# Kernel optimization log

Hardware: AMD Instinct MI355X
Metric: run time of the kernel (lower is better)

## Reference

```python
import jax, jax.numpy as jnp
import numpy as np

K = 7          # involution kernel size
PAD = 3        # (K-1)//2
G = 4          # groups = out_channels // group_channels
GC = 16        # group_channels
EPS = 1e-5     # BatchNorm eps


def _bn(x, g, b, m, v):
    # eval-mode BatchNorm2d over channel dim of NCHW
    scale = g / jnp.sqrt(v + EPS)
    return x * scale[:, None, None] + (b - m * scale)[:, None, None]


def _conv1x1(x, w, b=None):
    y = jnp.einsum('bchw,oc->bohw', x, w)
    if b is not None:
        y = y + b[:, None, None]
    return y


def _gelu(x):
    return jax.nn.gelu(x, approximate=False)  # torch nn.GELU default (erf)


def _involution(x, wr, gr, br, mr, vr, ws, bs):
    # kernel-generation branch: 1x1 reduce -> BN -> ReLU -> 1x1 span
    r = jax.nn.relu(_bn(_conv1x1(x, wr), gr, br, mr, vr))
    w = _conv1x1(r, ws, bs)                       # [B, G*K*K, H, W]
    B, _, H, W = w.shape
    w = w.reshape(B, G, K * K, H, W)
    # unfold x into KxK patches (channel-major then row-major kernel pos, matching nn.Unfold)
    xp = jnp.pad(x, ((0, 0), (0, 0), (PAD, PAD), (PAD, PAD)))
    patches = jnp.stack([xp[:, :, i:i + H, j:j + W]
                         for i in range(K) for j in range(K)], axis=2)  # [B, C, KK, H, W]
    patches = patches.reshape(B, G, GC, K * K, H, W)
    out = jnp.einsum('bgkhw,bgckhw->bgchw', w, patches)  # per-pixel dynamic kernel apply
    return out.reshape(B, G * GC, H, W)


def setup_inputs() -> dict:
    key = jax.random.key(0)
    ks = jax.random.split(key, 24)
    B, Cin, Cout, H, W = 4, 32, 64, 128, 128
    red = Cout // 4
    n = lambda k, s, sc: jax.random.normal(k, s, jnp.float32) * sc
    u = lambda k, s: jax.random.uniform(k, s, jnp.float32, 0.5, 1.5)
    inp = {
        'x': n(ks[0], (B, Cin, H, W), 1.0),
        'w1': n(ks[1], (Cout, Cin), 0.15),
        # involution: reduce conv + BN, span conv
        'wr': n(ks[2], (red, Cout), 0.12), 'gr': u(ks[3], (red,)), 'br': n(ks[4], (red,), 0.05),
        'mr': n(ks[5], (red,), 0.05), 'vr': u(ks[6], (red,)),
        'ws': n(ks[7], (K * K * G, red), 0.1), 'bs': n(ks[8], (K * K * G,), 0.02),
        # BN after involution
        'g1': u(ks[9], (Cout,)), 'b1': n(ks[10], (Cout,), 0.05),
        'm1': n(ks[11], (Cout,), 0.05), 'v1': u(ks[12], (Cout,)),
        # convblock2
        'w2': n(ks[13], (Cout, Cout), 0.12),
        'g2': u(ks[14], (Cout,)), 'b2': n(ks[15], (Cout,), 0.05),
        'm2': n(ks[16], (Cout,), 0.05), 'v2': u(ks[17], (Cout,)),
        # mapping (residual projection) conv has bias=True by default
        'wm': n(ks[18], (Cout, Cin), 0.15), 'bmap': n(ks[19], (Cout,), 0.02),
        'gm': u(ks[20], (Cout,)), 'betam': n(ks[21], (Cout,), 0.05),
        'mm': n(ks[22], (Cout,), 0.05), 'vm': u(ks[23], (Cout,)),
    }
    return inp


def reference(x, w1, wr, gr, br, mr, vr, ws, bs, g1, b1, m1, v1,
              w2, g2, b2, m2, v2, wm, bmap, gm, betam, mm, vm):
    x1 = _gelu(_conv1x1(x, w1))                                  # convblock
    x1 = _gelu(_bn(_involution(x1, wr, gr, br, mr, vr, ws, bs),
                   g1, b1, m1, v1))                              # involution + BN + GELU
    x1 = _bn(_conv1x1(x1, w2), g2, b2, m2, v2)                   # convblock2
    skip = _bn(_conv1x1(x, wm, bmap), gm, betam, mm, vm)         # mapping (Cin != Cout)
    return _gelu(x1 + skip)
```

## Files before the change

### kernel.cpp

```cpp
#include <hip/hip_runtime.h>
#include <hip/hip_bf16.h>
#include <math.h>

#define HW    16384
#define Bsz   4
#define CIN   32
#define COUT  64
#define RED   16
#define KKN   49
#define GG    4
#define PW    134
#define PPLANE (PW*PW)
#define N16PAD 574592

typedef __hip_bfloat16 bf16;
typedef __attribute__((ext_vector_type(8))) short bf16x8;
typedef __attribute__((ext_vector_type(4))) float f32x4;

__device__ __forceinline__ float gelu_f(float x) {
    return 0.5f * x * (1.0f + erff(x * 0.70710678118654752f));
}
__device__ __forceinline__ void unpack_bf2(unsigned u, float& lo, float& hi) {
    lo = __uint_as_float(u << 16);
    hi = __uint_as_float(u & 0xffff0000u);
}
__device__ __forceinline__ unsigned pack_bf2(float lo, float hi) {
    unsigned a = __float_as_uint(lo), b = __float_as_uint(hi);
    a += 0x7fff + ((a >> 16) & 1);
    b += 0x7fff + ((b >> 16) & 1);
    return (a >> 16) | (b & 0xffff0000u);
}
__device__ __forceinline__ unsigned short bf16r(float v) {
    unsigned a = __float_as_uint(v);
    a += 0x7fff + ((a >> 16) & 1);
    return (unsigned short)(a >> 16);
}

#define OFF_RBUF  9437184
#define OFF_X2B   13631488
#define OFF_PAR   22020096
#define OFF_XBF   22085632
#define PRSH_F 0
#define PSHC_F 16
#define PSMV_F 80
#define PSC1_F 144
#define PSH1_F 208
#define BW1B 4096
#define BWRB 8192
#define BCAT 12288

__global__ __launch_bounds__(256) void k0_init(
    const float* __restrict__ x,
    const float* __restrict__ w1, const float* __restrict__ wr,
    const float* __restrict__ gr, const float* __restrict__ br,
    const float* __restrict__ mr, const float* __restrict__ vr,
    const float* __restrict__ g1, const float* __restrict__ b1,
    const float* __restrict__ m1, const float* __restrict__ v1,
    const float* __restrict__ w2, const float* __restrict__ g2,
    const float* __restrict__ b2, const float* __restrict__ m2,
    const float* __restrict__ v2,
    const float* __restrict__ wm, const float* __restrict__ bmap,
    const float* __restrict__ gm, const float* __restrict__ betam,
    const float* __restrict__ mm, const float* __restrict__ vm,
    char* __restrict__ parb, uint4* __restrict__ x1pad,
    unsigned short* __restrict__ xbf, int nzb)
{
    int bid = blockIdx.x, t = threadIdx.x;
    if (bid >= 1 && bid <= nzb) {
        int i = (bid - 1) * 256 + t;
        if (i < N16PAD) x1pad[i] = make_uint4(0u, 0u, 0u, 0u);
        return;
    }
    if (bid > nzb) {
        int gpx = (bid - nzb - 1) * 256 + t;
        int b = gpx >> 14, p = gpx & (HW - 1);
        float xv[CIN];
#pragma unroll
        for (int c = 0; c < CIN; ++c) xv[c] = x[(b * CIN + c) * HW + p];
        unsigned pk[16];
#pragma unroll
        for (int d = 0; d < 16; ++d) pk[d] = pack_bf2(xv[2 * d], xv[2 * d + 1]);
        unsigned* xo = (unsigned*)&xbf[(size_t)gpx * 32];
        *(uint4*)xo        = make_uint4(pk[0], pk[1], pk[2], pk[3]);
        *(uint4*)(xo + 4)  = make_uint4(pk[4], pk[5], pk[6], pk[7]);
        *(uint4*)(xo + 8)  = make_uint4(pk[8], pk[9], pk[10], pk[11]);
        *(uint4*)(xo + 12) = make_uint4(pk[12], pk[13], pk[14], pk[15]);
        return;
    }
    float* parf = (float*)parb;
    unsigned short* w1b  = (unsigned short*)(parb + BW1B);
    unsigned short* wrb  = (unsigned short*)(parb + BWRB);
    unsigned short* wcat = (unsigned short*)(parb + BCAT);
    for (int i = t; i < 64 * 32; i += 256)
        w1b[i] = bf16r(w1[i]);
    for (int i = t; i < 16 * 64; i += 256) {
        int j = i >> 6;
        float sc = gr[j] * rsqrtf(vr[j] + 1e-5f);
        wrb[i] = bf16r(wr[i] * sc);
    }
    for (int i = t; i < 64 * 96; i += 256) {
        int o = i / 96, c = i - o * 96;
        float v;
        if (c < 64) {
            float s2 = g2[o] * rsqrtf(v2[o] + 1e-5f);
            float sm = gm[o] * rsqrtf(vm[o] + 1e-5f);
            v = w2[o * COUT + c] * (s2 / sm);
        } else {
            v = wm[o * CIN + (c - 64)];
        }
        wcat[i] = bf16r(v);
    }
    if (t < 16) {
        float sc = gr[t] * rsqrtf(vr[t] + 1e-5f);
        parf[PRSH_F + t] = br[t] - mr[t] * sc;
    }
    if (t < 64) {
        float s2 = g2[t] * rsqrtf(v2[t] + 1e-5f);
        float sm = gm[t] * rsqrtf(vm[t] + 1e-5f);
        parf[PSHC_F + t] = (b2[t] - m2[t] * s2) + (betam[t] + (bmap[t] - mm[t]) * sm);
        parf[PSMV_F + t] = sm;
        float s1 = g1[t] * rsqrtf(v1[t] + 1e-5f);
        parf[PSC1_F + t] = s1;
        parf[PSH1_F + t] = b1[t] - m1[t] * s1;
    }
}

__global__ __launch_bounds__(256, 4) void k1_mfma(
    const unsigned short* __restrict__ xbf, const char* __restrict__ parb,
    unsigned* __restrict__ x1pad, float* __restrict__ rbuf)
{
    __shared__ float x1f[4][16][65];

    int lane = threadIdx.x & 63;
    int wave = threadIdx.x >> 6;
    int m15 = lane & 15, quad = lane >> 4;
    int base_gpx = blockIdx.x * 64 + wave * 16;
    int b   = base_gpx >> 14;
    int px0 = base_gpx & (HW - 1);

    const unsigned short* w1b = (const unsigned short*)(parb + BW1B);
    const unsigned short* wrb = (const unsigned short*)(parb + BWRB);
    const float* parf = (const float*)parb;

    bf16x8 Af = *(const bf16x8*)&xbf[((size_t)(base_gpx + m15)) * 32 + quad * 8];
    f32x4 acc[4];
#pragma unroll
    for (int nt = 0; nt < 4; ++nt) {
        bf16x8 Bf = *(const bf16x8*)&w1b[(nt * 16 + m15) * 32 + quad * 8];
        f32x4 z = {0.f, 0.f, 0.f, 0.f};
        acc[nt] = __builtin_amdgcn_mfma_f32_16x16x32_bf16(Af, Bf, z, 0, 0, 0);
    }
#pragma unroll
    for (int nt = 0; nt < 4; ++nt)
#pragma unroll
        for (int reg = 0; reg < 4; ++reg)
            x1f[wave][quad * 4 + reg][nt * 16 + m15] = gelu_f(acc[nt][reg]);

    __syncthreads();

    {
        int pxl = lane >> 2, g = lane & 3;
        int p = px0 + pxl, h = p >> 7, w = p & 127;
        unsigned pk[8];
#pragma unroll
        for (int d = 0; d < 8; ++d)
            pk[d] = pack_bf2(x1f[wave][pxl][g * 16 + 2 * d],
                             x1f[wave][pxl][g * 16 + 2 * d + 1]);
        unsigned* xo = x1pad +
            ((size_t)((b * GG + g) * PW + (h + 3)) * PW + (w + 3)) * 8;
        *(uint4*)xo       = make_uint4(pk[0], pk[1], pk[2], pk[3]);
        *(uint4*)(xo + 4) = make_uint4(pk[4], pk[5], pk[6], pk[7]);
    }

    f32x4 racc = {0.f, 0.f, 0.f, 0.f};
#pragma unroll
    for (int kt = 0; kt < 2; ++kt) {
        bf16x8 A2, B2;
#pragma unroll
        for (int j = 0; j < 8; ++j)
            A2[j] = (short)bf16r(x1f[wave][m15][kt * 32 + quad * 8 + j]);
        B2 = *(const bf16x8*)&wrb[m15 * 64 + kt * 32 + quad * 8];
        racc = __builtin_amdgcn_mfma_f32_16x16x32_bf16(A2, B2, racc, 0, 0, 0);
    }
    float rsh = parf[PRSH_F + m15];
#pragma unroll
    for (int reg = 0; reg < 4; ++reg) {
        int gp = base_gpx + quad * 4 + reg;
        rbuf[(size_t)gp * 16 + m15] = fmaxf(racc[reg] + rsh, 0.f);
    }
}

__global__ __launch_bounds__(256, 4) void k23_involution(
    const unsigned* __restrict__ x1pad, const float* __restrict__ rbuf,
    const float* __restrict__ wsp, const float* __restrict__ bsp,
    const float* __restrict__ par, unsigned* __restrict__ x2b)
{
    int bg = blockIdx.x >> 6;
    int g = bg & 3, b = bg >> 2;
    int p = ((blockIdx.x & 63) << 8) + threadIdx.x;
    int h = p >> 7, w0 = p & 127;

    float r[RED];
    {
        const float4* rp = (const float4*)&rbuf[((size_t)b * HW + p) * 16];
        float4 r0 = rp[0], r1 = rp[1], r2 = rp[2], r3 = rp[3];
        r[0]=r0.x; r[1]=r0.y; r[2]=r0.z; r[3]=r0.w;
        r[4]=r1.x; r[5]=r1.y; r[6]=r1.z; r[7]=r1.w;
        r[8]=r2.x; r[9]=r2.y; r[10]=r2.z; r[11]=r2.w;
        r[12]=r3.x; r[13]=r3.y; r[14]=r3.z; r[15]=r3.w;
    }

    const float* wrow = wsp + g * KKN * RED;
    const float* brow = bsp + g * KKN;
    const unsigned* base = x1pad + ((size_t)(bg * PW + h) * PW + w0) * 8;

    float acc[RED];
#pragma unroll
    for (int c = 0; c < RED; ++c) acc[c] = 0.f;

#pragma unroll 1
    for (int i = 0; i < 7; ++i) {
#pragma unroll 1
        for (int j = 0; j < 7; ++j) {
            int k = i * 7 + j;
            const float* wk_row = wrow + k * RED;
            float s = brow[k];
#pragma unroll
            for (int jj = 0; jj < RED; ++jj) s += r[jj] * wk_row[jj];
            const unsigned* tp = base + (size_t)(i * PW + j) * 8;
            uint4 A = *(const uint4*)tp;
            uint4 B = *(const uint4*)(tp + 4);
            float lo, hi;
            unpack_bf2(A.x, lo, hi); acc[0] += s*lo; acc[1] += s*hi;
            unpack_bf2(A.y, lo, hi); acc[2] += s*lo; acc[3] += s*hi;
            unpack_bf2(A.z, lo, hi); acc[4] += s*lo; acc[5] += s*hi;
            unpack_bf2(A.w, lo, hi); acc[6] += s*lo; acc[7] += s*hi;
            unpack_bf2(B.x, lo, hi); acc[8] += s*lo; acc[9] += s*hi;
            unpack_bf2(B.y, lo, hi); acc[10]+= s*lo; acc[11]+= s*hi;
            unpack_bf2(B.z, lo, hi); acc[12]+= s*lo; acc[13]+= s*hi;
            unpack_bf2(B.w, lo, hi); acc[14]+= s*lo; acc[15]+= s*hi;
        }
    }

    unsigned pk[8];
#pragma unroll
    for (int d = 0; d < 8; ++d) {
        int ch0 = g * RED + 2 * d, ch1 = ch0 + 1;
        float v0 = gelu_f(par[PSC1_F + ch0] * acc[2 * d]     + par[PSH1_F + ch0]);
        float v1 = gelu_f(par[PSC1_F + ch1] * acc[2 * d + 1] + par[PSH1_F + ch1]);
        pk[d] = pack_bf2(v0, v1);
    }
    unsigned* xo = x2b + ((size_t)bg * HW + p) * 8;
    *(uint4*)xo       = make_uint4(pk[0], pk[1], pk[2], pk[3]);
    *(uint4*)(xo + 4) = make_uint4(pk[4], pk[5], pk[6], pk[7]);
}

__global__ __launch_bounds__(256, 4) void k4_mfma(
    const unsigned short* __restrict__ x2s, const unsigned short* __restrict__ xbf,
    const char* __restrict__ parb, float* __restrict__ out)
{
    int lane = threadIdx.x & 63;
    int wave = threadIdx.x >> 6;
    int m15  = lane & 15;
    int quad = lane >> 4;
    int b    = blockIdx.x >> 8;
    int px0  = (((blockIdx.x & 255) << 2) + wave) << 4;

    const unsigned short* wcat = (const unsigned short*)(parb + BCAT);
    const float* parf = (const float*)parb;

    bf16x8 Bf[3][4];
#pragma unroll
    for (int kt = 0; kt < 3; ++kt)
#pragma unroll
        for (int nt = 0; nt < 4; ++nt)
            Bf[kt][nt] = *(const bf16x8*)&wcat[(nt * 16 + m15) * 96 + kt * 32 + quad * 8];

    int px = px0 + m15;
    bf16x8 Af[3];
    {
        int g0 = quad >> 1, co = (quad & 1) * 8;
        Af[0] = *(const bf16x8*)&x2s[((size_t)((b * 4 + g0) * HW + px)) * 16 + co];
        Af[1] = *(const bf16x8*)&x2s[((size_t)((b * 4 + 2 + g0) * HW + px)) * 16 + co];
        Af[2] = *(const bf16x8*)&xbf[((size_t)(b * HW + px)) * 32 + quad * 8];
    }

    f32x4 acc[4];
#pragma unroll
    for (int nt = 0; nt < 4; ++nt) acc[nt] = (f32x4){0.f, 0.f, 0.f, 0.f};
#pragma unroll
    for (int kt = 0; kt < 3; ++kt)
#pragma unroll
        for (int nt = 0; nt < 4; ++nt)
            acc[nt] = __builtin_amdgcn_mfma_f32_16x16x32_bf16(
                Af[kt], Bf[kt][nt], acc[nt], 0, 0, 0);

#pragma unroll
    for (int nt = 0; nt < 4; ++nt) {
        int o = nt * 16 + m15;
        float smv = parf[PSMV_F + o], sh = parf[PSHC_F + o];
        float* op = out + (size_t)(b * COUT + o) * HW + px0 + quad * 4;
#pragma unroll
        for (int reg = 0; reg < 4; ++reg)
            op[reg] = gelu_f(smv * acc[nt][reg] + sh);
    }
}

extern "C" void kernel_launch(void* const* d_in, const int* in_sizes, int n_in,
                              void* d_out, int out_size, void* d_ws, size_t ws_size,
                              hipStream_t stream) {
    const float* x    = (const float*)d_in[0];
    const float* w1   = (const float*)d_in[1];
    const float* wr   = (const float*)d_in[2];
    const float* gr   = (const float*)d_in[3];
    const float* br   = (const float*)d_in[4];
    const float* mr   = (const float*)d_in[5];
    const float* vr   = (const float*)d_in[6];
    const float* wsp  = (const float*)d_in[7];
    const float* bsp  = (const float*)d_in[8];
    const float* g1   = (const float*)d_in[9];
    const float* b1   = (const float*)d_in[10];
    const float* m1   = (const float*)d_in[11];
    const float* v1   = (const float*)d_in[12];
    const float* w2   = (const float*)d_in[13];
    const float* g2   = (const float*)d_in[14];
    const float* b2   = (const float*)d_in[15];
    const float* m2   = (const float*)d_in[16];
    const float* v2   = (const float*)d_in[17];
    const float* wm   = (const float*)d_in[18];
    const float* bmap = (const float*)d_in[19];
    const float* gm   = (const float*)d_in[20];
    const float* betam= (const float*)d_in[21];
    const float* mm   = (const float*)d_in[22];
    const float* vm   = (const float*)d_in[23];

    unsigned*       x1pad = (unsigned*)d_ws;
    float*          rbuf  = (float*)((char*)d_ws + OFF_RBUF);
    unsigned*       x2b   = (unsigned*)((char*)d_ws + OFF_X2B);
    char*           parb  = (char*)d_ws + OFF_PAR;
    unsigned short* xbf   = (unsigned short*)((char*)d_ws + OFF_XBF);

    int nzb = (N16PAD + 255) / 256;
    int nxb = Bsz * HW / 256;
    k0_init<<<1 + nzb + nxb, 256, 0, stream>>>(
        x, w1, wr, gr, br, mr, vr, g1, b1, m1, v1,
        w2, g2, b2, m2, v2, wm, bmap, gm, betam, mm, vm,
        parb, (uint4*)x1pad, xbf, nzb);
    k1_mfma<<<Bsz * HW / 64, 256, 0, stream>>>(xbf, parb, x1pad, rbuf);
    k23_involution<<<Bsz * GG * HW / 256, 256, 0, stream>>>(
        x1pad, rbuf, wsp, bsp, (const float*)parb, x2b);
    k4_mfma<<<Bsz * HW / 64, 256, 0, stream>>>(
        (const unsigned short*)x2b, xbf, parb, (float*)d_out);
}
```

Measured before the change: 170.8 us.

## Fuse involution with final 1x1 conv via LDS and zero only halo

```diff
diff --git a/kernel.cpp b/kernel.cpp
--- a/kernel.cpp
+++ b/kernel.cpp
@@ -11,7 +11,7 @@
 #define GG    4
 #define PW    134
 #define PPLANE (PW*PW)
-#define N16PAD 574592
+#define NHALO 25152
 
 typedef __hip_bfloat16 bf16;
 typedef __attribute__((ext_vector_type(8))) short bf16x8;
@@ -67,8 +67,26 @@
 {
     int bid = blockIdx.x, t = threadIdx.x;
     if (bid >= 1 && bid <= nzb) {
-        int i = (bid - 1) * 256 + t;
-        if (i < N16PAD) x1pad[i] = make_uint4(0u, 0u, 0u, 0u);
+        unsigned i = (unsigned)(bid - 1) * 256u + (unsigned)t;
+        if (i < NHALO) {
+            unsigned plane = i / 1572u;
+            unsigned rem = i - plane * 1572u;
+            unsigned row, col;
+            if (rem < 804u) {
+                unsigned rr = rem / 134u;
+                col = rem - rr * 134u;
+                row = rr < 3u ? rr : rr + 128u;
+            } else {
+                unsigned r2 = rem - 804u;
+                unsigned rr = r2 / 6u;
+                unsigned cc = r2 - rr * 6u;
+                row = rr + 3u;
+                col = cc < 3u ? cc : cc + 128u;
+            }
+            uint4* q = x1pad + ((size_t)(plane * PW + row) * PW + col) * 2;
+            q[0] = make_uint4(0u, 0u, 0u, 0u);
+            q[1] = make_uint4(0u, 0u, 0u, 0u);
+        }
         return;
     }
     if (bid > nzb) {
@@ -190,119 +208,123 @@
     }
 }
 
-__global__ __launch_bounds__(256, 4) void k23_involution(
+__global__ __launch_bounds__(256, 4) void k34_fused(
     const unsigned* __restrict__ x1pad, const float* __restrict__ rbuf,
     const float* __restrict__ wsp, const float* __restrict__ bsp,
-    const float* __restrict__ par, unsigned* __restrict__ x2b)
+    const char* __restrict__ parb, const unsigned short* __restrict__ xbf,
+    float* __restrict__ out)
 {
-    int bg = blockIdx.x >> 6;
-    int g = bg & 3, b = bg >> 2;
-    int p = ((blockIdx.x & 63) << 8) + threadIdx.x;
-    int h = p >> 7, w0 = p & 127;
-
-    float r[RED];
+    __shared__ unsigned short x2t[64][88];
+
+    const float* par = (const float*)parb;
+    int t = threadIdx.x;
+    int b = blockIdx.x >> 8;
+    int pxblk = (blockIdx.x & 255) << 6;
+
     {
-        const float4* rp = (const float4*)&rbuf[((size_t)b * HW + p) * 16];
-        float4 r0 = rp[0], r1 = rp[1], r2 = rp[2], r3 = rp[3];
-        r[0]=r0.x; r[1]=r0.y; r[2]=r0.z; r[3]=r0.w;
-        r[4]=r1.x; r[5]=r1.y; r[6]=r1.z; r[7]=r1.w;
-        r[8]=r2.x; r[9]=r2.y; r[10]=r2.z; r[11]=r2.w;
-        r[12]=r3.x; r[13]=r3.y; r[14]=r3.z; r[15]=r3.w;
-    }
-
-    const float* wrow = wsp + g * KKN * RED;
-    const float* brow = bsp + g * KKN;
-    const unsigned* base = x1pad + ((size_t)(bg * PW + h) * PW + w0) * 8;
-
-    float acc[RED];
-#pragma unroll
-    for (int c = 0; c < RED; ++c) acc[c] = 0.f;
+        int pxl = t & 63;
+        int g = __builtin_amdgcn_readfirstlane(t >> 6);
+        int p = pxblk + pxl;
+        int h = p >> 7, w0 = p & 127;
+        int bg = b * GG + g;
+
+        float r[RED];
+        {
+            const float4* rp = (const float4*)&rbuf[((size_t)b * HW + p) * 16];
+            float4 r0 = rp[0], r1 = rp[1], r2 = rp[2], r3 = rp[3];
+            r[0]=r0.x; r[1]=r0.y; r[2]=r0.z; r[3]=r0.w;
+            r[4]=r1.x; r[5]=r1.y; r[6]=r1.z; r[7]=r1.w;
+            r[8]=r2.x; r[9]=r2.y; r[10]=r2.z; r[11]=r2.w;
+            r[12]=r3.x; r[13]=r3.y; r[14]=r3.z; r[15]=r3.w;
+        }
+
+        const float* wrow = wsp + g * KKN * RED;
+        const float* brow = bsp + g * KKN;
+        const unsigned* base = x1pad + ((size_t)(bg * PW + h) * PW + w0) * 8;
+
+        float acc[RED];
+#pragma unroll
+        for (int c = 0; c < RED; ++c) acc[c] = 0.f;
 
 #pragma unroll 1
-    for (int i = 0; i < 7; ++i) {
+        for (int i = 0; i < 7; ++i) {
 #pragma unroll 1
-        for (int j = 0; j < 7; ++j) {
-            int k = i * 7 + j;
-            const float* wk_row = wrow + k * RED;
-            float s = brow[k];
-#pragma unroll
-            for (int jj = 0; jj < RED; ++jj) s += r[jj] * wk_row[jj];
-            const unsigned* tp = base + (size_t)(i * PW + j) * 8;
-            uint4 A = *(const uint4*)tp;
-            uint4 B = *(const uint4*)(tp + 4);
-            float lo, hi;
-            unpack_bf2(A.x, lo, hi); acc[0] += s*lo; acc[1] += s*hi;
-            unpack_bf2(A.y, lo, hi); acc[2] += s*lo; acc[3] += s*hi;
-            unpack_bf2(A.z, lo, hi); acc[4] += s*lo; acc[5] += s*hi;
-            unpack_bf2(A.w, lo, hi); acc[6] += s*lo; acc[7] += s*hi;
-            unpack_bf2(B.x, lo, hi); acc[8] += s*lo; acc[9] += s*hi;
-            unpack_bf2(B.y, lo, hi); acc[10]+= s*lo; acc[11]+= s*hi;
-            unpack_bf2(B.z, lo, hi); acc[12]+= s*lo; acc[13]+= s*hi;
-            unpack_bf2(B.w, lo, hi); acc[14]+= s*lo; acc[15]+= s*hi;
-        }
-    }
-
-    unsigned pk[8];
-#pragma unroll
-    for (int d = 0; d < 8; ++d) {
-        int ch0 = g * RED + 2 * d, ch1 = ch0 + 1;
-        float v0 = gelu_f(par[PSC1_F + ch0] * acc[2 * d]     + par[PSH1_F + ch0]);
-        float v1 = gelu_f(par[PSC1_F + ch1] * acc[2 * d + 1] + par[PSH1_F + ch1]);
-        pk[d] = pack_bf2(v0, v1);
-    }
-    unsigned* xo = x2b + ((size_t)bg * HW + p) * 8;
-    *(uint4*)xo       = make_uint4(pk[0], pk[1], pk[2], pk[3]);
-    *(uint4*)(xo + 4) = make_uint4(pk[4], pk[5], pk[6], pk[7]);
-}
-
-__global__ __launch_bounds__(256, 4) void k4_mfma(
-    const unsigned short* __restrict__ x2s, const unsigned short* __restrict__ xbf,
-    const char* __restrict__ parb, float* __restrict__ out)
-{
-    int lane = threadIdx.x & 63;
-    int wave = threadIdx.x >> 6;
-    int m15  = lane & 15;
-    int quad = lane >> 4;
-    int b    = blockIdx.x >> 8;
-    int px0  = (((blockIdx.x & 255) << 2) + wave) << 4;
-
-    const unsigned short* wcat = (const unsigned short*)(parb + BCAT);
-    const float* parf = (const float*)parb;
-
-    bf16x8 Bf[3][4];
-#pragma unroll
-    for (int kt = 0; kt < 3; ++kt)
-#pragma unroll
-        for (int nt = 0; nt < 4; ++nt)
-            Bf[kt][nt] = *(const bf16x8*)&wcat[(nt * 16 + m15) * 96 + kt * 32 + quad * 8];
-
-    int px = px0 + m15;
-    bf16x8 Af[3];
+            for (int j = 0; j < 7; ++j) {
+                int k = i * 7 + j;
+                const float* wk_row = wrow + k * RED;
+                float s = brow[k];
+#pragma unroll
+                for (int jj = 0; jj < RED; ++jj) s += r[jj] * wk_row[jj];
+                const unsigned* tp = base + (size_t)(i * PW + j) * 8;
+                uint4 A = *(const uint4*)tp;
+                uint4 B = *(const uint4*)(tp + 4);
+                float lo, hi;
+                unpack_bf2(A.x, lo, hi); acc[0] += s*lo; acc[1] += s*hi;
+                unpack_bf2(A.y, lo, hi); acc[2] += s*lo; acc[3] += s*hi;
+                unpack_bf2(A.z, lo, hi); acc[4] += s*lo; acc[5] += s*hi;
+                unpack_bf2(A.w, lo, hi); acc[6] += s*lo; acc[7] += s*hi;
+                unpack_bf2(B.x, lo, hi); acc[8] += s*lo; acc[9] += s*hi;
+                unpack_bf2(B.y, lo, hi); acc[10]+= s*lo; acc[11]+= s*hi;
+                unpack_bf2(B.z, lo, hi); acc[12]+= s*lo; acc[13]+= s*hi;
+                unpack_bf2(B.w, lo, hi); acc[14]+= s*lo; acc[15]+= s*hi;
+            }
+        }
+
+        unsigned pk[8];
+#pragma unroll
+        for (int d = 0; d < 8; ++d) {
+            int ch0 = g * RED + 2 * d, ch1 = ch0 + 1;
+            float v0 = gelu_f(par[PSC1_F + ch0] * acc[2 * d]     + par[PSH1_F + ch0]);
+            float v1 = gelu_f(par[PSC1_F + ch1] * acc[2 * d + 1] + par[PSH1_F + ch1]);
+            pk[d] = pack_bf2(v0, v1);
+        }
+        unsigned* xo = (unsigned*)&x2t[pxl][g * RED];
+        *(uint4*)xo       = make_uint4(pk[0], pk[1], pk[2], pk[3]);
+        *(uint4*)(xo + 4) = make_uint4(pk[4], pk[5], pk[6], pk[7]);
+    }
+
+    __syncthreads();
+
     {
-        int g0 = quad >> 1, co = (quad & 1) * 8;
-        Af[0] = *(const bf16x8*)&x2s[((size_t)((b * 4 + g0) * HW + px)) * 16 + co];
-        Af[1] = *(const bf16x8*)&x2s[((size_t)((b * 4 + 2 + g0) * HW + px)) * 16 + co];
-        Af[2] = *(const bf16x8*)&xbf[((size_t)(b * HW + px)) * 32 + quad * 8];
-    }
-
-    f32x4 acc[4];
-#pragma unroll
-    for (int nt = 0; nt < 4; ++nt) acc[nt] = (f32x4){0.f, 0.f, 0.f, 0.f};
-#pragma unroll
-    for (int kt = 0; kt < 3; ++kt)
-#pragma unroll
-        for (int nt = 0; nt < 4; ++nt)
-            acc[nt] = __builtin_amdgcn_mfma_f32_16x16x32_bf16(
-                Af[kt], Bf[kt][nt], acc[nt], 0, 0, 0);
-
-#pragma unroll
-    for (int nt = 0; nt < 4; ++nt) {
-        int o = nt * 16 + m15;
-        float smv = parf[PSMV_F + o], sh = parf[PSHC_F + o];
-        float* op = out + (size_t)(b * COUT + o) * HW + px0 + quad * 4;
-#pragma unroll
-        for (int reg = 0; reg < 4; ++reg)
-            op[reg] = gelu_f(smv * acc[nt][reg] + sh);
+        int lane = t & 63, wave = t >> 6;
+        int m15  = lane & 15;
+        int quad = lane >> 4;
+        int pxl0 = wave * 16;
+        int px0  = pxblk + pxl0;
+
+        const unsigned short* wcat = (const unsigned short*)(parb + BCAT);
+
+        bf16x8 Bf[3][4];
+#pragma unroll
+        for (int kt = 0; kt < 3; ++kt)
+#pragma unroll
+            for (int nt = 0; nt < 4; ++nt)
+                Bf[kt][nt] = *(const bf16x8*)&wcat[(nt * 16 + m15) * 96 + kt * 32 + quad * 8];
+
+        bf16x8 Af[3];
+        Af[0] = *(const bf16x8*)&x2t[pxl0 + m15][quad * 8];
+        Af[1] = *(const bf16x8*)&x2t[pxl0 + m15][32 + quad * 8];
+        Af[2] = *(const bf16x8*)&xbf[((size_t)(b * HW + px0 + m15)) * 32 + quad * 8];
+
+        f32x4 acc[4];
+#pragma unroll
+        for (int nt = 0; nt < 4; ++nt) acc[nt] = (f32x4){0.f, 0.f, 0.f, 0.f};
+#pragma unroll
+        for (int kt = 0; kt < 3; ++kt)
+#pragma unroll
+            for (int nt = 0; nt < 4; ++nt)
+                acc[nt] = __builtin_amdgcn_mfma_f32_16x16x32_bf16(
+                    Af[kt], Bf[kt][nt], acc[nt], 0, 0, 0);
+
+#pragma unroll
+        for (int nt = 0; nt < 4; ++nt) {
+            int o = nt * 16 + m15;
+            float smv = par[PSMV_F + o], sh = par[PSHC_F + o];
+            float* op = out + (size_t)(b * COUT + o) * HW + px0 + quad * 4;
+#pragma unroll
+            for (int reg = 0; reg < 4; ++reg)
+                op[reg] = gelu_f(smv * acc[nt][reg] + sh);
+        }
     }
 }
 
@@ -336,19 +358,16 @@
 
     unsigned*       x1pad = (unsigned*)d_ws;
     float*          rbuf  = (float*)((char*)d_ws + OFF_RBUF);
-    unsigned*       x2b   = (unsigned*)((char*)d_ws + OFF_X2B);
     char*           parb  = (char*)d_ws + OFF_PAR;
     unsigned short* xbf   = (unsigned short*)((char*)d_ws + OFF_XBF);
 
-    int nzb = (N16PAD + 255) / 256;
+    int nzb = (NHALO + 255) / 256;
     int nxb = Bsz * HW / 256;
     k0_init<<<1 + nzb + nxb, 256, 0, stream>>>(
         x, w1, wr, gr, br, mr, vr, g1, b1, m1, v1,
         w2, g2, b2, m2, v2, wm, bmap, gm, betam, mm, vm,
         parb, (uint4*)x1pad, xbf, nzb);
     k1_mfma<<<Bsz * HW / 64, 256, 0, stream>>>(xbf, parb, x1pad, rbuf);
-    k23_involution<<<Bsz * GG * HW / 256, 256, 0, stream>>>(
-        x1pad, rbuf, wsp, bsp, (const float*)parb, x2b);
-    k4_mfma<<<Bsz * HW / 64, 256, 0, stream>>>(
-        (const unsigned short*)x2b, xbf, parb, (float*)d_out);
-}
+    k34_fused<<<Bsz * GG * HW / 256, 256, 0, stream>>>(
+        x1pad, rbuf, wsp, bsp, parb, xbf, (float*)d_out);
+}
```

Result: faster. 166.1 us (-2.8%).
